# Kernel tuning notes

Measured on AMD Instinct MI355X. Metric: run time of the kernel, lower is better.

## Reference

```python
import jax, jax.numpy as jnp
import numpy as np

N = 100000
E = 1600000
IN_DIM = 128
HID_DIM = 128
NUM_CLASSES = 40


def setup_inputs() -> dict:
    key = jax.random.key(0)
    k1, k2, k3, k4, k5, k6 = jax.random.split(key, 6)
    x = jax.random.normal(k1, (N, IN_DIM), dtype=jnp.float32)
    e = jax.random.randint(k2, (2, E), 0, N, dtype=jnp.int64)
    s1 = 1.0 / np.sqrt(IN_DIM)
    s2 = 1.0 / np.sqrt(HID_DIM)
    W1 = jax.random.uniform(k3, (IN_DIM, HID_DIM), jnp.float32, -s1, s1)
    b1 = jax.random.uniform(k4, (HID_DIM,), jnp.float32, -s1, s1)
    W2 = jax.random.uniform(k5, (HID_DIM, NUM_CLASSES), jnp.float32, -s2, s2)
    b2 = jax.random.uniform(k6, (NUM_CLASSES,), jnp.float32, -s2, s2)
    return {"x": x, "e": e, "W1": W1, "b1": b1, "W2": W2, "b2": b2}


def _gcn_conv(x, src, dst, norm, W, b, n):
    # linear transform first (PyG GCNConv), then normalized aggregation
    h = x @ W                                    # [N, d_out]
    out = jax.ops.segment_sum(h[src] * norm[:, None], dst, num_segments=n)
    return out + b


def reference(x, e, W1, b1, W2, b2):
    n = x.shape[0]
    loop = jnp.arange(n, dtype=e.dtype)
    src = jnp.concatenate([e[0], loop])          # add self-loops
    dst = jnp.concatenate([e[1], loop])
    deg = jax.ops.segment_sum(jnp.ones_like(dst, dtype=x.dtype), dst, num_segments=n)
    d_inv_sqrt = deg ** -0.5                     # deg >= 1 due to self-loops
    norm = d_inv_sqrt[src] * d_inv_sqrt[dst]     # symmetric normalization
    h = jax.nn.relu(_gcn_conv(x, src, dst, norm, W1, b1, n))
    return _gcn_conv(h, src, dst, norm, W2, b2, n)
```

## Files before the change

kernel.cpp:

```cpp
#include <hip/hip_runtime.h>


typedef unsigned int u32;
typedef unsigned short u16;
typedef __attribute__((ext_vector_type(8))) short short8;
typedef __attribute__((ext_vector_type(4))) float floatx4;

#define CHUNK 4096

static __device__ inline u16 f2bf(float f) {
    u32 u = __float_as_uint(f);
    return (u16)((u + 0x7FFFu + ((u >> 16) & 1u)) >> 16);
}
static __device__ inline u32 pack2(float a, float b) {
    return (u32)f2bf(a) | ((u32)f2bf(b) << 16);
}
static __device__ inline float bflo(u32 u) { return __uint_as_float(u << 16); }
static __device__ inline float bfhi(u32 u) { return __uint_as_float(u & 0xffff0000u); }

static __device__ inline bool detect_is64(const int* e32, int lane) {
    bool nz = e32[2 * lane + 1] != 0;
    return __ballot(nz) == 0ull;
}

__global__ void k_prepW(const float* __restrict__ W1, const float* __restrict__ W2,
                        u16* __restrict__ WTb, u16* __restrict__ W2Tb) {
    int id = blockIdx.x * 256 + threadIdx.x;
    if (id < 16384) {
        int k = id >> 7, c = id & 127;
        WTb[c * 128 + k] = f2bf(W1[id]);
    } else {
        int id2 = id - 16384;
        if (id2 < 6144) {
            int c = id2 >> 7, k = id2 & 127;
            W2Tb[id2] = f2bf(c < 40 ? W2[k * 40 + c] : 0.f);
        }
    }
}

__global__ __launch_bounds__(256) void k_front(const void* __restrict__ e_raw,
                                               int E, int NC, int NB,
                                               int* __restrict__ histG,
                                               const float* __restrict__ X,
                                               const u16* __restrict__ WTb,
                                               u16* __restrict__ H1s, int n) {
    __shared__ u32 smem[64 * 68 + 128 * 68];
    const int tid = threadIdx.x;
    if ((int)blockIdx.x < NC) {
        int* h = (int*)smem;
        h[tid] = 0; h[tid + 256] = 0;
        __syncthreads();
        const int* e32 = (const int*)e_raw;
        bool is64 = detect_is64(e32, tid & 63);
        int c = blockIdx.x;
        int j0 = c * CHUNK, j1 = min(E, j0 + CHUNK);
        for (int j = j0 + tid; j < j1; j += 256) {
            int d = is64 ? (int)((const long long*)e_raw)[E + j] : e32[E + j];
            atomicAdd(&h[d >> 8], 1);
        }
        __syncthreads();
        for (int b = tid; b < NB; b += 256) histG[(size_t)b * NC + c] = h[b];
        return;
    }
    u32* As = smem;
    u32* Bs = smem + 64 * 68;
    const int row0 = ((int)blockIdx.x - NC) * 64;
#pragma unroll
    for (int it = 0; it < 8; it++) {
        int i = tid + it * 256;
        int r = i >> 5;
        int c4 = (i & 31) << 2;
        int gr = row0 + r;
        float4 v = make_float4(0.f, 0.f, 0.f, 0.f);
        if (gr < n) v = *(const float4*)(X + (size_t)gr * 128 + c4);
        uint2 p;
        p.x = pack2(v.x, v.y);
        p.y = pack2(v.z, v.w);
        *(uint2*)&As[r * 68 + (c4 >> 1)] = p;
    }
#pragma unroll
    for (int it = 0; it < 8; it++) {
        int i = tid + it * 256;
        int r = i >> 4;
        int c4 = (i & 15) << 2;
        *(uint4*)&Bs[r * 68 + c4] =
            *(const uint4*)((const u32*)WTb + (size_t)r * 64 + c4);
    }
    __syncthreads();

    const int lane = tid & 63;
    const int wave = tid >> 6;
    const int wr = wave >> 1;
    const int wc = wave & 1;
    const int mrow = lane & 15;
    const int quad = lane >> 4;

    floatx4 acc[2][4] = {};
    for (int k0 = 0; k0 < 128; k0 += 32) {
        int koff = (k0 >> 1) + quad * 4;
        short8 a[2], b[4];
#pragma unroll
        for (int i = 0; i < 2; i++)
            a[i] = *(const short8*)&As[((wr * 2 + i) * 16 + mrow) * 68 + koff];
#pragma unroll
        for (int j = 0; j < 4; j++)
            b[j] = *(const short8*)&Bs[((wc * 4 + j) * 16 + mrow) * 68 + koff];
#pragma unroll
        for (int i = 0; i < 2; i++)
#pragma unroll
            for (int j = 0; j < 4; j++)
                acc[i][j] = __builtin_amdgcn_mfma_f32_16x16x32_bf16(
                    a[i], b[j], acc[i][j], 0, 0, 0);
    }
#pragma unroll
    for (int i = 0; i < 2; i++) {
        int gr0 = row0 + (wr * 2 + i) * 16 + quad * 4;
#pragma unroll
        for (int j = 0; j < 4; j++) {
            int gcol = (wc * 4 + j) * 16 + mrow;
#pragma unroll
            for (int rg = 0; rg < 4; rg++) {
                int grow = gr0 + rg;
                if (grow < n)
                    H1s[(size_t)grow * 128 + gcol] = f2bf(acc[i][j][rg]);
            }
        }
    }
}

__global__ void k_scan1(const int* __restrict__ in, int* __restrict__ out,
                        int* __restrict__ bsum, int n) {
    __shared__ int sh[256];
    int i = blockIdx.x * 256 + threadIdx.x;
    int v = (i < n) ? in[i] : 0;
    sh[threadIdx.x] = v;
    __syncthreads();
    for (int off = 1; off < 256; off <<= 1) {
        int t = (threadIdx.x >= off) ? sh[threadIdx.x - off] : 0;
        __syncthreads();
        sh[threadIdx.x] += t;
        __syncthreads();
    }
    if (i < n) out[i] = sh[threadIdx.x] - v;
    if (threadIdx.x == 255) bsum[blockIdx.x] = sh[255];
}

__global__ void k_scan2(int* __restrict__ bsum, int nb) {
    __shared__ int sh[1024];
    int t = threadIdx.x;
    int v = (t < nb) ? bsum[t] : 0;
    sh[t] = v;
    __syncthreads();
    for (int off = 1; off < 1024; off <<= 1) {
        int u = (t >= off) ? sh[t - off] : 0;
        __syncthreads();
        sh[t] += u;
        __syncthreads();
    }
    if (t < nb) bsum[t] = sh[t] - v;
}

__global__ __launch_bounds__(256) void k_place(const void* __restrict__ e_raw,
                                               const int* __restrict__ histOff,
                                               const int* __restrict__ bsumH,
                                               u32* __restrict__ tmp,
                                               int E, int NB, int NC) {
    __shared__ int cur[512];
    int c = blockIdx.x;
    int t = threadIdx.x;
    for (int b = t; b < NB; b += 256) {
        int idx = b * NC + c;
        cur[b] = histOff[idx] + bsumH[idx >> 8];
    }
    __syncthreads();
    const int* e32 = (const int*)e_raw;
    bool is64 = detect_is64(e32, t & 63);
    int j0 = c * CHUNK, j1 = min(E, j0 + CHUNK);
    for (int j = j0 + t; j < j1; j += 256) {
        int s, d;
        if (is64) {
            s = (int)((const long long*)e_raw)[j];
            d = (int)((const long long*)e_raw)[E + j];
        } else {
            s = e32[j];
            d = e32[E + j];
        }
        int pos = atomicAdd(&cur[d >> 8], 1);
        tmp[pos] = (u32)s | ((u32)(d & 255) << 24);
    }
}

__global__ __launch_bounds__(256) void k_degsort(const u32* __restrict__ tmp,
                                                 const int* __restrict__ histOff,
                                                 const int* __restrict__ bsumH,
                                                 int* __restrict__ degI,
                                                 float* __restrict__ dinv,
                                                 int* __restrict__ rs,
                                                 int* __restrict__ eSrc,
                                                 int n, int NB, int NC, int E) {
    __shared__ int cnt[256];
    __shared__ int sh[256];
    __shared__ int cur[256];
    int b = blockIdx.x;
    int t = threadIdx.x;
    cnt[t] = 0;
    __syncthreads();
    int i0 = b * NC;
    int seg0 = histOff[i0] + bsumH[i0 >> 8];
    int seg1 = E;
    if (b + 1 < NB) {
        int i1 = (b + 1) * NC;
        seg1 = histOff[i1] + bsumH[i1 >> 8];
    }
    for (int j = seg0 + t; j < seg1; j += 256) atomicAdd(&cnt[tmp[j] >> 24], 1);
    __syncthreads();
    int v = cnt[t];
    sh[t] = v;
    __syncthreads();
    for (int off = 1; off < 256; off <<= 1) {
        int u = (t >= off) ? sh[t - off] : 0;
        __syncthreads();
        sh[t] += u;
        __syncthreads();
    }
    int myStart = seg0 + sh[t] - v;
    cur[t] = myStart;
    int node = b * 256 + t;
    if (node < n) {
        degI[node] = v;
        dinv[node] = rsqrtf((float)v + 1.0f);
        rs[node] = myStart;
    }
    __syncthreads();
    for (int j = seg0 + t; j < seg1; j += 256) {
        u32 rec = tmp[j];
        int dl = rec >> 24;
        int s = (int)(rec & 0x00FFFFFFu);
        int pos = atomicAdd(&cur[dl], 1);
        eSrc[pos] = s;
    }
}

__global__ __launch_bounds__(256) void k_gather128(
    const u32* __restrict__ Hb, const int* __restrict__ rs,
    const int* __restrict__ degI, const int* __restrict__ eSrc,
    const float* __restrict__ dinv, const float* __restrict__ b1,
    u32* __restrict__ outb, int n) {
    int wave = threadIdx.x >> 6;
    int lane = threadIdx.x & 63;
    int node = blockIdx.x * 4 + wave;
    if (node >= n) return;
    int start = rs[node];
    int deg = degI[node];
    float ax = 0.f, ay = 0.f;
    for (int base = 0; base < deg; base += 64) {
        int mS = 0;
        float mW = 0.f;
        if (base + lane < deg) { mS = eSrc[start + base + lane]; mW = dinv[mS]; }
        int cnt = min(64, deg - base);
        int t = 0;
        for (; t + 16 <= cnt; t += 16) {
            int ss[16];
            float ww[16];
            u32 uu[16];
#pragma unroll
            for (int q = 0; q < 16; q++) {
                ss[q] = __shfl(mS, t + q);
                ww[q] = __shfl(mW, t + q);
            }
#pragma unroll
            for (int q = 0; q < 16; q++) uu[q] = Hb[(size_t)ss[q] * 64 + lane];
#pragma unroll
            for (int q = 0; q < 16; q++) {
                ax = fmaf(ww[q], bflo(uu[q]), ax);
                ay = fmaf(ww[q], bfhi(uu[q]), ay);
            }
        }
        for (; t + 4 <= cnt; t += 4) {
            int s0 = __shfl(mS, t + 0), s1 = __shfl(mS, t + 1);
            int s2 = __shfl(mS, t + 2), s3 = __shfl(mS, t + 3);
            float w0 = __shfl(mW, t + 0), w1 = __shfl(mW, t + 1);
            float w2 = __shfl(mW, t + 2), w3 = __shfl(mW, t + 3);
            u32 u0 = Hb[(size_t)s0 * 64 + lane];
            u32 u1 = Hb[(size_t)s1 * 64 + lane];
            u32 u2 = Hb[(size_t)s2 * 64 + lane];
            u32 u3 = Hb[(size_t)s3 * 64 + lane];
            ax = fmaf(w0, bflo(u0), ax); ay = fmaf(w0, bfhi(u0), ay);
            ax = fmaf(w1, bflo(u1), ax); ay = fmaf(w1, bfhi(u1), ay);
            ax = fmaf(w2, bflo(u2), ax); ay = fmaf(w2, bfhi(u2), ay);
            ax = fmaf(w3, bflo(u3), ax); ay = fmaf(w3, bfhi(u3), ay);
        }
        for (; t < cnt; t++) {
            int s = __shfl(mS, t);
            float w = __shfl(mW, t);
            u32 u = Hb[(size_t)s * 64 + lane];
            ax = fmaf(w, bflo(u), ax); ay = fmaf(w, bfhi(u), ay);
        }
    }
    float di = dinv[node];
    u32 us = Hb[(size_t)node * 64 + lane];
    float inx = fmaf(di, bflo(us), ax);
    float iny = fmaf(di, bfhi(us), ay);
    float2 bv = *(const float2*)(b1 + lane * 2);
    float rx = fmaxf(fmaf(di, inx, bv.x), 0.f);
    float ry = fmaxf(fmaf(di, iny, bv.y), 0.f);
    outb[(size_t)node * 64 + lane] = pack2(rx, ry);
}

__global__ __launch_bounds__(256) void k_gemm2(const u32* __restrict__ A1b,
                                               const u16* __restrict__ W2Tb,
                                               const float* __restrict__ dinv,
                                               u16* __restrict__ H2s, int n) {
    __shared__ u32 As[64 * 68];
    __shared__ u32 Bs[48 * 68];
    const int tid = threadIdx.x;
    const int row0 = blockIdx.x * 64;
#pragma unroll
    for (int it = 0; it < 4; it++) {
        int i = tid + it * 256;
        int r = i >> 4;
        int c4 = (i & 15) << 2;
        int gr = row0 + r;
        uint4 v = make_uint4(0u, 0u, 0u, 0u);
        if (gr < n) v = *(const uint4*)(A1b + (size_t)gr * 64 + c4);
        *(uint4*)&As[r * 68 + c4] = v;
    }
#pragma unroll
    for (int it = 0; it < 3; it++) {
        int i = tid + it * 256;
        int r = i >> 4;
        int c4 = (i & 15) << 2;
        *(uint4*)&Bs[r * 68 + c4] =
            *(const uint4*)((const u32*)W2Tb + (size_t)r * 64 + c4);
    }
    __syncthreads();

    const int lane = tid & 63;
    const int wave = tid >> 6;
    const int mrow = lane & 15;
    const int quad = lane >> 4;

    floatx4 acc[3] = {};
    for (int k0 = 0; k0 < 128; k0 += 32) {
        int koff = (k0 >> 1) + quad * 4;
        short8 a = *(const short8*)&As[(wave * 16 + mrow) * 68 + koff];
#pragma unroll
        for (int j = 0; j < 3; j++) {
            short8 b = *(const short8*)&Bs[(j * 16 + mrow) * 68 + koff];
            acc[j] = __builtin_amdgcn_mfma_f32_16x16x32_bf16(a, b, acc[j], 0, 0, 0);
        }
    }
    int gr0 = row0 + wave * 16 + quad * 4;
    float dv[4];
#pragma unroll
    for (int rg = 0; rg < 4; rg++)
        dv[rg] = (gr0 + rg < n) ? dinv[gr0 + rg] : 0.f;
#pragma unroll
    for (int j = 0; j < 3; j++) {
        int gcol = j * 16 + mrow;
        if (gcol < 40) {
#pragma unroll
            for (int rg = 0; rg < 4; rg++) {
                int grow = gr0 + rg;
                if (grow < n)
                    H2s[(size_t)grow * 40 + gcol] = f2bf(dv[rg] * acc[j][rg]);
            }
        }
    }
}

__global__ __launch_bounds__(256) void k_gather40(
    const u32* __restrict__ H2b, const int* __restrict__ rs,
    const int* __restrict__ degI, const int* __restrict__ eSrc,
    const float* __restrict__ dinv, const float* __restrict__ b2,
    float* __restrict__ out, int n) {
    int wave = threadIdx.x >> 6;
    int lane = threadIdx.x & 63;
    int node = blockIdx.x * 4 + wave;
    if (node >= n) return;
    int start = rs[node];
    int deg = degI[node];
    int g = lane / 20;
    int l = lane - g * 20;
    float ax = 0.f, ay = 0.f;
    for (int base = 0; base < deg; base += 64) {
        int mS = 0;
        if (base + lane < deg) mS = eSrc[start + base + lane];
        int cnt = min(64, deg - base);
        for (int t = 0; t < cnt; t += 12) {
            int i0 = t + g, i1 = t + 3 + g, i2 = t + 6 + g, i3 = t + 9 + g;
            int s0 = __shfl(mS, i0 & 63), s1 = __shfl(mS, i1 & 63);
            int s2 = __shfl(mS, i2 & 63), s3 = __shfl(mS, i3 & 63);
            bool v0 = (g < 3) && (i0 < cnt), v1 = (g < 3) && (i1 < cnt);
            bool v2 = (g < 3) && (i2 < cnt), v3 = (g < 3) && (i3 < cnt);
            u32 u0 = H2b[(size_t)s0 * 20 + l];
            u32 u1 = H2b[(size_t)s1 * 20 + l];
            u32 u2 = H2b[(size_t)s2 * 20 + l];
            u32 u3 = H2b[(size_t)s3 * 20 + l];
            if (v0) { ax += bflo(u0); ay += bfhi(u0); }
            if (v1) { ax += bflo(u1); ay += bfhi(u1); }
            if (v2) { ax += bflo(u2); ay += bfhi(u2); }
            if (v3) { ax += bflo(u3); ay += bfhi(u3); }
        }
    }
    float x1 = __shfl(ax, (lane + 20) & 63), y1 = __shfl(ay, (lane + 20) & 63);
    float x2 = __shfl(ax, (lane + 40) & 63), y2 = __shfl(ay, (lane + 40) & 63);
    if (lane < 20) {
        float di = dinv[node];
        u32 u = H2b[(size_t)node * 20 + l];
        float2 bv = *(const float2*)(b2 + l * 2);
        float ox = fmaf(di, ax + x1 + x2 + bflo(u), bv.x);
        float oy = fmaf(di, ay + y1 + y2 + bfhi(u), bv.y);
        *(float2*)(out + (size_t)node * 40 + l * 2) = make_float2(ox, oy);
    }
}

extern "C" void kernel_launch(void* const* d_in, const int* in_sizes, int n_in,
                              void* d_out, int out_size, void* d_ws, size_t ws_size,
                              hipStream_t stream) {
    const float* x  = (const float*)d_in[0];
    const void*  e  = d_in[1];
    const float* W1 = (const float*)d_in[2];
    const float* b1 = (const float*)d_in[3];
    const float* W2 = (const float*)d_in[4];
    const float* b2 = (const float*)d_in[5];
    float* out = (float*)d_out;

    const int n = in_sizes[0] / 128;
    const int E = in_sizes[1] / 2;
    const int NB = (n + 255) / 256;
    const int NC = (E + CHUNK - 1) / CHUNK;
    const int NH = NB * NC;
    const int nbH = (NH + 255) / 256;
    const int G1 = (n + 63) / 64;

    int*   degI    = (int*)d_ws;
    int*   rs      = degI + n;
    int*   bsumH   = rs + n;
    float* dinv    = (float*)(bsumH + 1024);
    int*   histG   = (int*)(dinv + n);
    int*   histOff = histG + NH;
    size_t off = (size_t)((char*)(histOff + NH) - (char*)d_ws);
    off = (off + 15) & ~(size_t)15;
    u16*   WTb    = (u16*)((char*)d_ws + off);
    u16*   W2Tb   = WTb + 16384;
    off = (size_t)((char*)(W2Tb + 6144) - (char*)d_ws);
    off = (off + 15) & ~(size_t)15;
    u32*   tmp    = (u32*)((char*)d_ws + off);
    int*   eSrc   = (int*)(tmp + (size_t)E);
    u16*   H1s    = (u16*)(eSrc + (size_t)E);
    u32*   H1b    = (u32*)H1s;
    u32*   A1b    = (u32*)(H1s + (size_t)n * 128);
    u16*   H2s    = (u16*)(A1b + (size_t)n * 64);
    u32*   H2b    = (u32*)H2s;

    k_prepW<<<88, 256, 0, stream>>>(W1, W2, WTb, W2Tb);
    k_front<<<NC + G1, 256, 0, stream>>>(e, E, NC, NB, histG, x, WTb, H1s, n);

    k_scan1<<<nbH, 256, 0, stream>>>(histG, histOff, bsumH, NH);
    k_scan2<<<1, 1024, 0, stream>>>(bsumH, nbH);
    k_place<<<NC, 256, 0, stream>>>(e, histOff, bsumH, tmp, E, NB, NC);

    k_degsort<<<NB, 256, 0, stream>>>(tmp, histOff, bsumH, degI, dinv, rs,
                                      eSrc, n, NB, NC, E);

    k_gather128<<<(n + 3) / 4, 256, 0, stream>>>(H1b, rs, degI, eSrc, dinv,
                                                 b1, A1b, n);
    k_gemm2<<<(n + 63) / 64, 256, 0, stream>>>(A1b, W2Tb, dinv, H2s, n);
    k_gather40<<<(n + 3) / 4, 256, 0, stream>>>(H2b, rs, degI, eSrc, dinv,
                                                b2, out, n);
}
```

Measured before the change: 305.6 us.

## Split hidden features into two column planes and gather each plane separately

The GEMM1 output and the layer-1 aggregate are stored as two planes of 64 bf16 columns each instead of 128-column rows. The gather kernel now processes one 128-byte plane row per edge, with half-waves handling alternating edges, and it runs twice, once per plane. Each plane is 12.8 MB, so the random gathers get a smaller working set that should fit better in L2/MALL. The cost is reading the edge lists twice, extra shuffles, a cross-half reduction and a partial-edge tail loop.

```diff
diff --git a/kernel.cpp b/kernel.cpp
--- a/kernel.cpp
+++ b/kernel.cpp
@@ -118,11 +118,14 @@
 #pragma unroll
         for (int j = 0; j < 4; j++) {
             int gcol = (wc * 4 + j) * 16 + mrow;
+            int p = gcol >> 6;
+            int cc = gcol & 63;
 #pragma unroll
             for (int rg = 0; rg < 4; rg++) {
                 int grow = gr0 + rg;
                 if (grow < n)
-                    H1s[(size_t)grow * 128 + gcol] = f2bf(acc[i][j][rg]);
+                    H1s[(size_t)p * (size_t)n * 64 + (size_t)grow * 64 + cc] =
+                        f2bf(acc[i][j][rg]);
             }
         }
     }
@@ -241,13 +244,15 @@
     }
 }
 
-__global__ __launch_bounds__(256) void k_gather128(
-    const u32* __restrict__ Hb, const int* __restrict__ rs,
+__global__ __launch_bounds__(256) void k_gatherH(
+    const u32* __restrict__ Hp, const int* __restrict__ rs,
     const int* __restrict__ degI, const int* __restrict__ eSrc,
-    const float* __restrict__ dinv, const float* __restrict__ b1,
-    u32* __restrict__ outb, int n) {
+    const float* __restrict__ dinv, const float* __restrict__ b1p,
+    u32* __restrict__ outp, int n) {
     int wave = threadIdx.x >> 6;
     int lane = threadIdx.x & 63;
+    int half = lane >> 5;
+    int sub  = lane & 31;
     int node = blockIdx.x * 4 + wave;
     if (node >= n) return;
     int start = rs[node];
@@ -260,51 +265,44 @@
         int cnt = min(64, deg - base);
         int t = 0;
         for (; t + 16 <= cnt; t += 16) {
-            int ss[16];
-            float ww[16];
-            u32 uu[16];
-#pragma unroll
-            for (int q = 0; q < 16; q++) {
-                ss[q] = __shfl(mS, t + q);
-                ww[q] = __shfl(mW, t + q);
+            int ss[8];
+            float ww[8];
+            u32 uu[8];
+#pragma unroll
+            for (int q = 0; q < 8; q++) {
+                int e = t + 2 * q + half;
+                ss[q] = __shfl(mS, e);
+                ww[q] = __shfl(mW, e);
             }
 #pragma unroll
-            for (int q = 0; q < 16; q++) uu[q] = Hb[(size_t)ss[q] * 64 + lane];
-#pragma unroll
-            for (int q = 0; q < 16; q++) {
+            for (int q = 0; q < 8; q++) uu[q] = Hp[(size_t)ss[q] * 32 + sub];
+#pragma unroll
+            for (int q = 0; q < 8; q++) {
                 ax = fmaf(ww[q], bflo(uu[q]), ax);
                 ay = fmaf(ww[q], bfhi(uu[q]), ay);
             }
         }
-        for (; t + 4 <= cnt; t += 4) {
-            int s0 = __shfl(mS, t + 0), s1 = __shfl(mS, t + 1);
-            int s2 = __shfl(mS, t + 2), s3 = __shfl(mS, t + 3);
-            float w0 = __shfl(mW, t + 0), w1 = __shfl(mW, t + 1);
-            float w2 = __shfl(mW, t + 2), w3 = __shfl(mW, t + 3);
-            u32 u0 = Hb[(size_t)s0 * 64 + lane];
-            u32 u1 = Hb[(size_t)s1 * 64 + lane];
-            u32 u2 = Hb[(size_t)s2 * 64 + lane];
-            u32 u3 = Hb[(size_t)s3 * 64 + lane];
-            ax = fmaf(w0, bflo(u0), ax); ay = fmaf(w0, bfhi(u0), ay);
-            ax = fmaf(w1, bflo(u1), ax); ay = fmaf(w1, bfhi(u1), ay);
-            ax = fmaf(w2, bflo(u2), ax); ay = fmaf(w2, bfhi(u2), ay);
-            ax = fmaf(w3, bflo(u3), ax); ay = fmaf(w3, bfhi(u3), ay);
-        }
-        for (; t < cnt; t++) {
-            int s = __shfl(mS, t);
-            float w = __shfl(mW, t);
-            u32 u = Hb[(size_t)s * 64 + lane];
-            ax = fmaf(w, bflo(u), ax); ay = fmaf(w, bfhi(u), ay);
-        }
-    }
-    float di = dinv[node];
-    u32 us = Hb[(size_t)node * 64 + lane];
-    float inx = fmaf(di, bflo(us), ax);
-    float iny = fmaf(di, bfhi(us), ay);
-    float2 bv = *(const float2*)(b1 + lane * 2);
-    float rx = fmaxf(fmaf(di, inx, bv.x), 0.f);
-    float ry = fmaxf(fmaf(di, iny, bv.y), 0.f);
-    outb[(size_t)node * 64 + lane] = pack2(rx, ry);
+        for (; t < cnt; t += 2) {
+            int e = t + half;
+            int s = __shfl(mS, e & 63);
+            float w = (e < cnt) ? __shfl(mW, e & 63) : 0.f;
+            u32 u = Hp[(size_t)s * 32 + sub];
+            ax = fmaf(w, bflo(u), ax);
+            ay = fmaf(w, bfhi(u), ay);
+        }
+    }
+    ax += __shfl(ax, lane ^ 32);
+    ay += __shfl(ay, lane ^ 32);
+    if (lane < 32) {
+        float di = dinv[node];
+        u32 us = Hp[(size_t)node * 32 + sub];
+        float inx = fmaf(di, bflo(us), ax);
+        float iny = fmaf(di, bfhi(us), ay);
+        float2 bv = *(const float2*)(b1p + sub * 2);
+        float rx = fmaxf(fmaf(di, inx, bv.x), 0.f);
+        float ry = fmaxf(fmaf(di, iny, bv.y), 0.f);
+        outp[(size_t)node * 32 + sub] = pack2(rx, ry);
+    }
 }
 
 __global__ __launch_bounds__(256) void k_gemm2(const u32* __restrict__ A1b,
@@ -315,14 +313,18 @@
     __shared__ u32 Bs[48 * 68];
     const int tid = threadIdx.x;
     const int row0 = blockIdx.x * 64;
+    const size_t plane = (size_t)n * 32;
 #pragma unroll
     for (int it = 0; it < 4; it++) {
         int i = tid + it * 256;
         int r = i >> 4;
         int c4 = (i & 15) << 2;
+        int p = c4 >> 5;
+        int cc = c4 & 31;
         int gr = row0 + r;
         uint4 v = make_uint4(0u, 0u, 0u, 0u);
-        if (gr < n) v = *(const uint4*)(A1b + (size_t)gr * 64 + c4);
+        if (gr < n) v = *(const uint4*)(A1b + (size_t)p * plane +
+                                        (size_t)gr * 32 + cc);
         *(uint4*)&As[r * 68 + c4] = v;
     }
 #pragma unroll
@@ -450,9 +452,10 @@
     int*   eSrc   = (int*)(tmp + (size_t)E);
     u16*   H1s    = (u16*)(eSrc + (size_t)E);
     u32*   H1b    = (u32*)H1s;
-    u32*   A1b    = (u32*)(H1s + (size_t)n * 128);
-    u16*   H2s    = (u16*)(A1b + (size_t)n * 64);
+    u32*   A1b    = H1b + (size_t)2 * n * 32;
+    u16*   H2s    = (u16*)(A1b + (size_t)2 * n * 32);
     u32*   H2b    = (u32*)H2s;
+    const size_t plane = (size_t)n * 32;
 
     k_prepW<<<88, 256, 0, stream>>>(W1, W2, WTb, W2Tb);
     k_front<<<NC + G1, 256, 0, stream>>>(e, E, NC, NB, histG, x, WTb, H1s, n);
@@ -464,8 +467,11 @@
     k_degsort<<<NB, 256, 0, stream>>>(tmp, histOff, bsumH, degI, dinv, rs,
                                       eSrc, n, NB, NC, E);
 
-    k_gather128<<<(n + 3) / 4, 256, 0, stream>>>(H1b, rs, degI, eSrc, dinv,
-                                                 b1, A1b, n);
+    k_gatherH<<<(n + 3) / 4, 256, 0, stream>>>(H1b, rs, degI, eSrc, dinv,
+                                               b1, A1b, n);
+    k_gatherH<<<(n + 3) / 4, 256, 0, stream>>>(H1b + plane, rs, degI, eSrc,
+                                               dinv, b1 + 64, A1b + plane, n);
+
     k_gemm2<<<(n + 63) / 64, 256, 0, stream>>>(A1b, W2Tb, dinv, H2s, n);
     k_gather40<<<(n + 3) / 4, 256, 0, stream>>>(H2b, rs, degI, eSrc, dinv,
                                                 b2, out, n);
```

After: 338.8 us. +10.9%, slower.
